# Optimization experiments

Measured on AMD Instinct MI355X. Metric: run time of the kernel, lower is better.

Reference implementation:

```python
import jax, jax.numpy as jnp
import numpy as np

N, E, R, F, HD = 4096, 2048, 4, 128, 256
DEG_EPS = 1e-8
BN_EPS = 1e-5
LN_EPS = 1e-5


def _xavier(k, shape):
    scale = np.sqrt(2.0 / (shape[-2] + shape[-1])).astype(np.float32)
    return jax.random.normal(k, shape, jnp.float32) * scale


def setup_inputs() -> dict:
    key = jax.random.key(0)
    ks = jax.random.split(key, 8)
    X = jax.random.normal(ks[0], (N, F), jnp.float32)
    # sparse binary incidence matrices, one per relation type, stacked [R,N,E]
    H = (jax.random.uniform(ks[1], (R, N, E)) < 0.05).astype(jnp.float32)
    return {
        "X": X,
        "H": H,
        "W1": _xavier(ks[2], (R, F, HD)),
        "W2": _xavier(ks[3], (R, HD, HD)),
        "W3": _xavier(ks[4], (R, HD, F)),
        "imp": jnp.ones((3, R), jnp.float32),        # relation_importance per conv layer
        "b1": jnp.zeros((HD,), jnp.float32),
        "b2": jnp.zeros((HD,), jnp.float32),
        "b3": jnp.zeros((F,), jnp.float32),
        "bn_gamma": jnp.ones((2, HD), jnp.float32),
        "bn_beta": jnp.zeros((2, HD), jnp.float32),
        "ln_gamma": jnp.ones((2, HD), jnp.float32),
        "ln_beta": jnp.zeros((2, HD), jnp.float32),
        "rel_attn": jnp.ones((R,), jnp.float32) / R,
    }


def typed_conv(X, Hw, W, imp, bias):
    # Hw: [R,N,E] weighted incidence; theta = Dv^{-1/2} H De^{-1/2} via row/col scaling
    dv = jnp.power(Hw.sum(axis=2) + DEG_EPS, -0.5)   # [R,N]
    de = jnp.power(Hw.sum(axis=1) + DEG_EPS, -0.5)   # [R,E]
    theta = Hw * dv[:, :, None] * de[:, None, :]     # [R,N,E]
    # (theta @ theta^T) @ X computed as theta @ (theta^T @ X) -- same math, no NxN
    t = jnp.einsum('rne,nf->ref', theta, X)          # [R,E,Fin]
    Hn = jnp.einsum('rne,ref->rnf', theta, t)        # [R,N,Fin]
    out = jnp.einsum('rnf,rfo->rno', Hn, W)          # [R,N,Fout]
    out = out * jax.nn.sigmoid(imp)[:, None, None]
    return out.sum(axis=0) + bias


def bn_ln_elu(X, bg, bb, lg, lb):
    # BatchNorm1d with batch statistics (biased var), then LayerNorm, then ELU
    mu = X.mean(axis=0)
    var = X.var(axis=0)
    X = (X - mu) * jax.lax.rsqrt(var + BN_EPS) * bg + bb
    m = X.mean(axis=-1, keepdims=True)
    v = X.var(axis=-1, keepdims=True)
    X = (X - m) * jax.lax.rsqrt(v + LN_EPS) * lg + lb
    return jax.nn.elu(X)


def reference(X, H, W1, W2, W3, imp, b1, b2, b3, bn_gamma, bn_beta, ln_gamma, ln_beta, rel_attn):
    rw = jax.nn.softmax(rel_attn)
    Hw = H * rw[:, None, None]                       # weighted incidence per relation
    h = typed_conv(X, Hw, W1, imp[0], b1)
    h = bn_ln_elu(h, bn_gamma[0], bn_beta[0], ln_gamma[0], ln_beta[0])
    h = typed_conv(h, Hw, W2, imp[1], b2)
    h = bn_ln_elu(h, bn_gamma[1], bn_beta[1], ln_gamma[1], ln_beta[1])
    out = typed_conv(h, Hw, W3, imp[2], b3)
    return out + X  # residual: out_channels == in_channels by construction
```

## Files before the change

kernel.cpp:

```cpp
#include <hip/hip_runtime.h>
#include <hip/hip_bf16.h>

#define NN 4096
#define EE 2048
#define RR 4
#define FF 128
#define HDD 256

typedef __attribute__((ext_vector_type(4))) float floatx4;
typedef __attribute__((ext_vector_type(8))) __bf16 bf16x8;

#define AS1 __attribute__((address_space(1)))
#define AS3 __attribute__((address_space(3)))

__device__ __forceinline__ void async16(const void* g, void* l) {
  __builtin_amdgcn_global_load_lds((const AS1 void*)(unsigned long long)(g),
                                   (AS3 void*)(unsigned int)(unsigned long long)(l),
                                   16, 0, 0);
}

__device__ inline unsigned short f2b(float x) {
  unsigned int u = __float_as_uint(x);
  unsigned int r = u + 0x7fffu + ((u >> 16) & 1u);
  return (unsigned short)(r >> 16);
}
__device__ inline float b2f(unsigned short u) { return __uint_as_float((unsigned int)u << 16); }

__device__ inline float rel_w(const float* rel, int r) {
  float m = fmaxf(fmaxf(rel[0], rel[1]), fmaxf(rel[2], rel[3]));
  float s = 0.f;
#pragma unroll
  for (int i = 0; i < RR; i++) s += expf(rel[i] - m);
  return expf(rel[r] - m) / s;
}

__global__ void k_dvmask(const float* __restrict__ H, const float* __restrict__ rel,
                         float* __restrict__ dvs, unsigned long long* __restrict__ mask) {
  int wave = (blockIdx.x << 2) | (threadIdx.x >> 6);
  int lane = threadIdx.x & 63;
  int r = wave >> 12;
  const float* row = H + (size_t)wave * EE;
  unsigned long long* mrow = mask + (size_t)wave * (EE / 64);
  float s = 0.f;
  for (int j = 0; j < EE / 64; j++) {
    float h = row[j * 64 + lane];
    s += h;
    unsigned long long m = __ballot(h != 0.0f);
    if (lane == 0) mrow[j] = m;
  }
  for (int off = 32; off; off >>= 1) s += __shfl_down(s, off);
  if (lane == 0) {
    float rwr = rel_w(rel, r);
    dvs[wave] = rwr * rsqrtf(rwr * s + 1e-8f);
  }
}

__global__ void k_de_pop(const unsigned long long* __restrict__ mask, float* __restrict__ de_acc) {
  int wid = threadIdx.x >> 6, lane = threadIdx.x & 63;
  int wcol = blockIdx.x, r = blockIdx.z;
  int n0 = (blockIdx.y << 8) + (wid << 6);
  unsigned long long w = mask[(size_t)(r * NN + n0 + lane) * (EE / 64) + wcol];
  float cnt = 0.f;
#pragma unroll
  for (int b = 0; b < 64; b++) {
    unsigned long long m = __ballot(((w >> b) & 1ULL) != 0);
    if (lane == b) cnt = (float)__popcll(m);
  }
  atomicAdd(&de_acc[r * EE + (wcol << 6) + lane], cnt);
}

__global__ void k_build_theta_bits(const unsigned long long* __restrict__ mask,
                                   const float* __restrict__ dvs, const float* __restrict__ decnt,
                                   const float* __restrict__ rel,
                                   unsigned short* __restrict__ theta, unsigned short* __restrict__ thetaT) {
  __shared__ unsigned short tile[64][65];
  int r = blockIdx.z;
  int e0 = blockIdx.x * 64, n0 = blockIdx.y * 64;
  int tr = threadIdx.x >> 4, tc = threadIdx.x & 15;
  float rwr = rel_w(rel, r);
  float de0 = rsqrtf(rwr * decnt[r * EE + e0 + tc * 4 + 0] + 1e-8f);
  float de1 = rsqrtf(rwr * decnt[r * EE + e0 + tc * 4 + 1] + 1e-8f);
  float de2 = rsqrtf(rwr * decnt[r * EE + e0 + tc * 4 + 2] + 1e-8f);
  float de3 = rsqrtf(rwr * decnt[r * EE + e0 + tc * 4 + 3] + 1e-8f);
  int wcol = e0 >> 6;
#pragma unroll
  for (int i = 0; i < 4; i++) {
    int n = n0 + tr + 16 * i;
    unsigned long long w = mask[((size_t)r * NN + n) * (EE / 64) + wcol];
    float d = dvs[r * NN + n];
    unsigned short b0 = ((w >> (tc * 4 + 0)) & 1) ? f2b(d * de0) : 0;
    unsigned short b1 = ((w >> (tc * 4 + 1)) & 1) ? f2b(d * de1) : 0;
    unsigned short b2 = ((w >> (tc * 4 + 2)) & 1) ? f2b(d * de2) : 0;
    unsigned short b3 = ((w >> (tc * 4 + 3)) & 1) ? f2b(d * de3) : 0;
    ushort4 o; o.x = b0; o.y = b1; o.z = b2; o.w = b3;
    *(ushort4*)(theta + ((size_t)r * NN + n) * EE + e0 + tc * 4) = o;
    tile[tr + 16 * i][tc * 4 + 0] = b0;
    tile[tr + 16 * i][tc * 4 + 1] = b1;
    tile[tr + 16 * i][tc * 4 + 2] = b2;
    tile[tr + 16 * i][tc * 4 + 3] = b3;
  }
  __syncthreads();
#pragma unroll
  for (int i = 0; i < 4; i++) {
    int e = e0 + tr + 16 * i;
    ushort4 o;
    o.x = tile[tc * 4 + 0][tr + 16 * i];
    o.y = tile[tc * 4 + 1][tr + 16 * i];
    o.z = tile[tc * 4 + 2][tr + 16 * i];
    o.w = tile[tc * 4 + 3][tr + 16 * i];
    *(ushort4*)(thetaT + ((size_t)r * EE + e) * NN + n0 + tc * 4) = o;
  }
}

__global__ void k_cvtT(const float* __restrict__ src, unsigned short* __restrict__ dst, int M, int C) {
  __shared__ unsigned short tile[64][65];
  int c0 = blockIdx.x * 64, m0 = blockIdx.y * 64;
  int tr = threadIdx.x >> 4, tc = threadIdx.x & 15;
#pragma unroll
  for (int i = 0; i < 4; i++) {
    int m = m0 + tr + 16 * i;
    float4 v = *(const float4*)(src + (size_t)m * C + c0 + tc * 4);
    tile[tr + 16 * i][tc * 4 + 0] = f2b(v.x);
    tile[tr + 16 * i][tc * 4 + 1] = f2b(v.y);
    tile[tr + 16 * i][tc * 4 + 2] = f2b(v.z);
    tile[tr + 16 * i][tc * 4 + 3] = f2b(v.w);
  }
  __syncthreads();
#pragma unroll
  for (int i = 0; i < 4; i++) {
    int c = c0 + tr + 16 * i;
    ushort4 v;
    v.x = tile[tc * 4 + 0][tr + 16 * i];
    v.y = tile[tc * 4 + 1][tr + 16 * i];
    v.z = tile[tc * 4 + 2][tr + 16 * i];
    v.w = tile[tc * 4 + 3][tr + 16 * i];
    *(ushort4*)(dst + (size_t)c * M + m0 + tc * 4) = v;
  }
}

__global__ void k_trz(const unsigned short* __restrict__ src, unsigned short* __restrict__ dst, int M, int C) {
  __shared__ unsigned short tile[64][65];
  int c0 = blockIdx.x * 64, m0 = blockIdx.y * 64;
  int tr = threadIdx.x >> 4, tc = threadIdx.x & 15;
#pragma unroll
  for (int i = 0; i < 4; i++) {
    int m = m0 + tr + 16 * i;
    ushort4 v = *(const ushort4*)(src + (size_t)m * C + c0 + tc * 4);
    tile[tr + 16 * i][tc * 4 + 0] = v.x;
    tile[tr + 16 * i][tc * 4 + 1] = v.y;
    tile[tr + 16 * i][tc * 4 + 2] = v.z;
    tile[tr + 16 * i][tc * 4 + 3] = v.w;
  }
  __syncthreads();
#pragma unroll
  for (int i = 0; i < 4; i++) {
    int c = c0 + tr + 16 * i;
    ushort4 v;
    v.x = tile[tc * 4 + 0][tr + 16 * i];
    v.y = tile[tc * 4 + 1][tr + 16 * i];
    v.z = tile[tc * 4 + 2][tr + 16 * i];
    v.w = tile[tc * 4 + 3][tr + 16 * i];
    *(ushort4*)(dst + (size_t)c * M + m0 + tc * 4) = v;
  }
}

__global__ void k_wprep(const float* __restrict__ W1, const float* __restrict__ W2,
                        const float* __restrict__ W3, const float* __restrict__ imp,
                        unsigned short* __restrict__ W1catT, unsigned short* __restrict__ W2T,
                        unsigned short* __restrict__ W3T) {
  int idx = blockIdx.x * 256 + threadIdx.x;
  if (idx < RR * FF * HDD) {
    int o = idx % HDD, f = (idx / HDD) % FF, r = idx / (HDD * FF);
    float sg = 1.0f / (1.0f + expf(-imp[r]));
    W1catT[(size_t)o * (RR * FF) + r * FF + f] = f2b(sg * W1[((size_t)r * FF + f) * HDD + o]);
  } else if (idx < RR * FF * HDD + RR * HDD * HDD) {
    int j = idx - RR * FF * HDD;
    int c = j % HDD, o = (j / HDD) % HDD, r = j / (HDD * HDD);
    float sg = 1.0f / (1.0f + expf(-imp[RR + r]));
    W2T[j] = f2b(sg * W2[((size_t)r * HDD + c) * HDD + o]);
  } else {
    int j = idx - RR * FF * HDD - RR * HDD * HDD;
    int c = j % HDD, o = (j / HDD) % FF, r = j / (HDD * FF);
    float sg = 1.0f / (1.0f + expf(-imp[2 * RR + r]));
    W3T[j] = f2b(sg * W3[((size_t)r * HDD + c) * FF + o]);
  }
}

__global__ __launch_bounds__(256) void k_gemm3(
    const unsigned short* __restrict__ A, const unsigned short* __restrict__ BT,
    int K, int SK, int lda, int ldb, long a_rs, long b_rs,
    unsigned short* __restrict__ P, long c_ps, int ldc) {
  __shared__ unsigned short Al[128 * 64];
  __shared__ unsigned short Bl[128 * 64];
  int tid = threadIdx.x, wid = tid >> 6, lane = tid & 63;
  int m0 = blockIdx.x << 7, n0 = blockIdx.y << 7;
  int z = blockIdx.z, zr = z / SK, kz = z - zr * SK;
  int Kc = K / SK;
  int r8 = lane >> 3, c8 = lane & 7;
  int swz = ((c8 ^ r8) << 3);
  const unsigned short* Ab = A + (size_t)zr * a_rs + (size_t)m0 * lda + (size_t)kz * Kc;
  const unsigned short* Bb = BT + (size_t)zr * b_rs + (size_t)n0 * ldb + (size_t)kz * Kc;
  int wm = (wid >> 1) << 6, wn = (wid & 1) << 6;
  int fm = lane & 15, quad = lane >> 4;
  int f7 = fm & 7;
  floatx4 acc[4][4];
#pragma unroll
  for (int i = 0; i < 4; i++)
#pragma unroll
    for (int j = 0; j < 4; j++) acc[i][j] = (floatx4){0.f, 0.f, 0.f, 0.f};
  for (int k0 = 0; k0 < Kc; k0 += 64) {
#pragma unroll
    for (int t = 0; t < 4; t++) {
      int rbase = (wid << 5) + (t << 3);
      int row = rbase + r8;
      async16(Ab + (size_t)row * lda + k0 + swz, &Al[rbase * 64 + lane * 8]);
      async16(Bb + (size_t)row * ldb + k0 + swz, &Bl[rbase * 64 + lane * 8]);
    }
    __syncthreads();
#pragma unroll
    for (int ks = 0; ks < 2; ks++) {
      int kg = (ks << 2) | quad;
      int ko = ((kg ^ f7) << 3);
      bf16x8 a[4], b[4];
#pragma unroll
      for (int i = 0; i < 4; i++) {
        a[i] = *(const bf16x8*)&Al[(wm + i * 16 + fm) * 64 + ko];
        b[i] = *(const bf16x8*)&Bl[(wn + i * 16 + fm) * 64 + ko];
      }
#pragma unroll
      for (int i = 0; i < 4; i++)
#pragma unroll
        for (int j = 0; j < 4; j++)
          acc[i][j] = __builtin_amdgcn_mfma_f32_16x16x32_bf16(a[i], b[j], acc[i][j], 0, 0, 0);
    }
    __syncthreads();
  }
  unsigned short* Cb = P + (size_t)z * c_ps;
#pragma unroll
  for (int mi = 0; mi < 4; mi++)
#pragma unroll
    for (int ni = 0; ni < 4; ni++)
#pragma unroll
      for (int v = 0; v < 4; v++) {
        int row = m0 + wm + mi * 16 + quad * 4 + v;
        int col = n0 + wn + ni * 16 + fm;
        Cb[(size_t)row * ldc + col] = f2b(acc[mi][ni][v]);
      }
}

__global__ void k_red_b(const unsigned short* __restrict__ P, unsigned short* __restrict__ out,
                        int SK, long region) {
  long i = ((long)blockIdx.x * 256 + threadIdx.x) * 8;
  int zr = blockIdx.y;
  const unsigned short* p = P + (size_t)zr * SK * region + i;
  float s[8] = {0, 0, 0, 0, 0, 0, 0, 0};
  for (int k = 0; k < SK; k++) {
    const unsigned short* q = p + (size_t)k * region;
    ushort4 a = *(const ushort4*)q;
    ushort4 b = *(const ushort4*)(q + 4);
    s[0] += b2f(a.x); s[1] += b2f(a.y); s[2] += b2f(a.z); s[3] += b2f(a.w);
    s[4] += b2f(b.x); s[5] += b2f(b.y); s[6] += b2f(b.z); s[7] += b2f(b.w);
  }
  ushort4 o0, o1;
  o0.x = f2b(s[0]); o0.y = f2b(s[1]); o0.z = f2b(s[2]); o0.w = f2b(s[3]);
  o1.x = f2b(s[4]); o1.y = f2b(s[5]); o1.z = f2b(s[6]); o1.w = f2b(s[7]);
  unsigned short* d = out + (size_t)zr * region + i;
  *(ushort4*)d = o0;
  *(ushort4*)(d + 4) = o1;
}

__global__ void k_redT_b(const unsigned short* __restrict__ P, unsigned short* __restrict__ outT,
                         int SK, int M, int C) {
  __shared__ unsigned short tile[64][65];
  int zr = blockIdx.z;
  long region = (long)M * C;
  const unsigned short* p0 = P + (size_t)zr * SK * region;
  int c0 = blockIdx.x * 64, m0 = blockIdx.y * 64;
  int tr = threadIdx.x >> 4, tc = threadIdx.x & 15;
#pragma unroll
  for (int i = 0; i < 4; i++) {
    int m = m0 + tr + 16 * i;
    const unsigned short* p = p0 + (size_t)m * C + c0 + tc * 4;
    float s0 = 0, s1 = 0, s2 = 0, s3 = 0;
    for (int k = 0; k < SK; k++) {
      ushort4 v = *(const ushort4*)(p + (size_t)k * region);
      s0 += b2f(v.x); s1 += b2f(v.y); s2 += b2f(v.z); s3 += b2f(v.w);
    }
    tile[tr + 16 * i][tc * 4 + 0] = f2b(s0);
    tile[tr + 16 * i][tc * 4 + 1] = f2b(s1);
    tile[tr + 16 * i][tc * 4 + 2] = f2b(s2);
    tile[tr + 16 * i][tc * 4 + 3] = f2b(s3);
  }
  __syncthreads();
  unsigned short* d = outT + (size_t)zr * region;
#pragma unroll
  for (int i = 0; i < 4; i++) {
    int c = c0 + tr + 16 * i;
    ushort4 v;
    v.x = tile[tc * 4 + 0][tr + 16 * i];
    v.y = tile[tc * 4 + 1][tr + 16 * i];
    v.z = tile[tc * 4 + 2][tr + 16 * i];
    v.w = tile[tc * 4 + 3][tr + 16 * i];
    *(ushort4*)(d + (size_t)c * M + m0 + tc * 4) = v;
  }
}

__global__ void k_red_hcatb(const unsigned short* __restrict__ P, unsigned short* __restrict__ out, int SK) {
  long i = ((long)blockIdx.x * 256 + threadIdx.x) * 8;
  int r = blockIdx.y;
  const unsigned short* p = P + (size_t)r * SK * (NN * FF) + i;
  float s[8] = {0, 0, 0, 0, 0, 0, 0, 0};
  for (int k = 0; k < SK; k++) {
    const unsigned short* q = p + (size_t)k * (NN * FF);
    ushort4 a = *(const ushort4*)q;
    ushort4 b = *(const ushort4*)(q + 4);
    s[0] += b2f(a.x); s[1] += b2f(a.y); s[2] += b2f(a.z); s[3] += b2f(a.w);
    s[4] += b2f(b.x); s[5] += b2f(b.y); s[6] += b2f(b.z); s[7] += b2f(b.w);
  }
  long n = i >> 7;
  int f = (int)(i & 127);
  ushort4 o0, o1;
  o0.x = f2b(s[0]); o0.y = f2b(s[1]); o0.z = f2b(s[2]); o0.w = f2b(s[3]);
  o1.x = f2b(s[4]); o1.y = f2b(s[5]); o1.z = f2b(s[6]); o1.w = f2b(s[7]);
  unsigned short* d = out + n * (RR * FF) + r * FF + f;
  *(ushort4*)d = o0;
  *(ushort4*)(d + 4) = o1;
}

__global__ void k_redstats(const unsigned short* __restrict__ P, float* __restrict__ out,
                           float* __restrict__ cs, float* __restrict__ cs2, int Z) {
  __shared__ float sm[2][8][256];
  int cg = (threadIdx.x & 31) << 3;
  int rowt = threadIdx.x >> 5;
  int r0 = blockIdx.x * 32;
  float s[8] = {0, 0, 0, 0, 0, 0, 0, 0}, s2[8] = {0, 0, 0, 0, 0, 0, 0, 0};
  for (int j = 0; j < 4; j++) {
    long idx = (long)(r0 + rowt * 4 + j) * HDD + cg;
    float acc[8] = {0, 0, 0, 0, 0, 0, 0, 0};
    for (int z = 0; z < Z; z++) {
      const unsigned short* p = P + (size_t)z * ((long)NN * HDD) + idx;
      ushort4 a = *(const ushort4*)p;
      ushort4 b = *(const ushort4*)(p + 4);
      acc[0] += b2f(a.x); acc[1] += b2f(a.y); acc[2] += b2f(a.z); acc[3] += b2f(a.w);
      acc[4] += b2f(b.x); acc[5] += b2f(b.y); acc[6] += b2f(b.z); acc[7] += b2f(b.w);
    }
    float4 o0 = {acc[0], acc[1], acc[2], acc[3]};
    float4 o1 = {acc[4], acc[5], acc[6], acc[7]};
    *(float4*)(out + idx) = o0;
    *(float4*)(out + idx + 4) = o1;
#pragma unroll
    for (int i = 0; i < 8; i++) { s[i] += acc[i]; s2[i] += acc[i] * acc[i]; }
  }
#pragma unroll
  for (int i = 0; i < 8; i++) { sm[0][rowt][cg + i] = s[i]; sm[1][rowt][cg + i] = s2[i]; }
  __syncthreads();
  int c = threadIdx.x;
  float a0 = 0, a1 = 0;
#pragma unroll
  for (int t = 0; t < 8; t++) { a0 += sm[0][t][c]; a1 += sm[1][t][c]; }
  atomicAdd(&cs[c], a0);
  atomicAdd(&cs2[c], a1);
}

__global__ void k_red_out(const unsigned short* __restrict__ P, const float* __restrict__ X,
                          const float* __restrict__ b3, float* __restrict__ out, int Z) {
  long i = ((long)blockIdx.x * 256 + threadIdx.x) * 4;
  int f = (int)(i & 127);
  float4 s = *(const float4*)(X + i);
  s.x += b3[f]; s.y += b3[f + 1]; s.z += b3[f + 2]; s.w += b3[f + 3];
  for (int z = 0; z < Z; z++) {
    ushort4 v = *(const ushort4*)(P + (size_t)z * (NN * FF) + i);
    s.x += b2f(v.x); s.y += b2f(v.y); s.z += b2f(v.z); s.w += b2f(v.w);
  }
  *(float4*)(out + i) = s;
}

__global__ void k_bnlnelu(const float* __restrict__ x, const float* __restrict__ cs, const float* __restrict__ cs2,
                          const float* __restrict__ bg, const float* __restrict__ bb,
                          const float* __restrict__ lg, const float* __restrict__ lb,
                          unsigned short* __restrict__ out) {
  int wid = threadIdx.x >> 6, lane = threadIdx.x & 63;
  int n = blockIdx.x * 4 + wid;
  float y[4];
  float m = 0.f;
#pragma unroll
  for (int j = 0; j < 4; j++) {
    int c = lane + 64 * j;
    float mu = cs[c] * (1.0f / NN);
    float var = cs2[c] * (1.0f / NN) - mu * mu;
    float xv = x[(size_t)n * HDD + c];
    y[j] = (xv - mu) * rsqrtf(var + 1e-5f) * bg[c] + bb[c];
    m += y[j];
  }
  for (int off = 32; off; off >>= 1) m += __shfl_down(m, off);
  m = __shfl(m, 0) * (1.0f / HDD);
  float var = 0.f;
#pragma unroll
  for (int j = 0; j < 4; j++) { float d = y[j] - m; var += d * d; }
  for (int off = 32; off; off >>= 1) var += __shfl_down(var, off);
  var = __shfl(var, 0) * (1.0f / HDD);
  float inv = rsqrtf(var + 1e-5f);
#pragma unroll
  for (int j = 0; j < 4; j++) {
    int c = lane + 64 * j;
    float z = (y[j] - m) * inv * lg[c] + lb[c];
    z = z > 0.f ? z : expm1f(z);
    out[(size_t)n * HDD + c] = f2b(z);
  }
}

extern "C" void kernel_launch(void* const* d_in, const int* in_sizes, int n_in,
                              void* d_out, int out_size, void* d_ws, size_t ws_size,
                              hipStream_t stream) {
  const float* X   = (const float*)d_in[0];
  const float* H   = (const float*)d_in[1];
  const float* W1  = (const float*)d_in[2];
  const float* W2  = (const float*)d_in[3];
  const float* W3  = (const float*)d_in[4];
  const float* imp = (const float*)d_in[5];
  const float* b3  = (const float*)d_in[8];
  const float* bng = (const float*)d_in[9];
  const float* bnb = (const float*)d_in[10];
  const float* lng = (const float*)d_in[11];
  const float* lnb = (const float*)d_in[12];
  const float* rel = (const float*)d_in[13];
  (void)in_sizes; (void)n_in; (void)out_size; (void)ws_size;

  char* w = (char*)d_ws;
  size_t off = 0;
  auto alloc = [&](size_t bytes) -> void* {
    void* p = w + off;
    off += (bytes + 255) & ~(size_t)255;
    return p;
  };
  float* dvs  = (float*)alloc((size_t)RR * NN * 4);
  float* de   = (float*)alloc((size_t)RR * EE * 4);
  float* cs   = (float*)alloc(2 * HDD * 4);
  unsigned long long* mask = (unsigned long long*)alloc((size_t)RR * NN * (EE / 64) * 8);
  unsigned short* theta  = (unsigned short*)alloc((size_t)RR * NN * EE * 2);
  unsigned short* thetaT = (unsigned short*)alloc((size_t)RR * NN * EE * 2);
  unsigned short* bufP = (unsigned short*)alloc((size_t)16 * NN * HDD * 2);
  unsigned short* bufC = (unsigned short*)alloc((size_t)RR * EE * HDD * 2);
  unsigned short* bufD = (unsigned short*)alloc((size_t)RR * EE * HDD * 2);
  unsigned short* bufE = (unsigned short*)alloc((size_t)RR * EE * HDD * 2);
  float* convout = (float*)alloc((size_t)NN * HDD * 4);
  unsigned short* Xb  = (unsigned short*)alloc((size_t)NN * HDD * 2);
  unsigned short* XbT = (unsigned short*)alloc((size_t)NN * HDD * 2);
  unsigned short* W1catT = (unsigned short*)alloc((size_t)RR * FF * HDD * 2);
  unsigned short* W2T    = (unsigned short*)alloc((size_t)RR * HDD * HDD * 2);
  unsigned short* W3T    = (unsigned short*)alloc((size_t)RR * HDD * FF * 2);

  k_dvmask<<<(RR * NN) / 4, 256, 0, stream>>>(H, rel, dvs, mask);
  hipMemsetAsync(de, 0, (size_t)RR * EE * 4, stream);
  k_de_pop<<<dim3(EE / 64, NN / 256, RR), 256, 0, stream>>>(mask, de);
  k_build_theta_bits<<<dim3(EE / 64, NN / 64, RR), 256, 0, stream>>>(mask, dvs, de, rel, theta, thetaT);
  k_cvtT<<<dim3(FF / 64, NN / 64), 256, 0, stream>>>(X, XbT, NN, FF);
  k_wprep<<<(RR * FF * HDD + RR * HDD * HDD + RR * HDD * FF) / 256, 256, 0, stream>>>(
      W1, W2, W3, imp, W1catT, W2T, W3T);

  k_gemm3<<<dim3(1, EE / 128, RR * 8), 256, 0, stream>>>(
      XbT, thetaT, NN, 8, NN, NN, 0, (long)EE * NN, bufP, (long)FF * EE, EE);
  k_red_b<<<dim3((FF * EE) / 2048, RR), 256, 0, stream>>>(bufP, bufC, 8, (long)FF * EE);
  k_gemm3<<<dim3(NN / 128, 1, RR * 2), 256, 0, stream>>>(
      theta, bufC, EE, 2, EE, EE, (long)NN * EE, (long)FF * EE, bufP, (long)NN * FF, FF);
  k_red_hcatb<<<dim3((NN * FF) / 2048, RR), 256, 0, stream>>>(bufP, bufD, 2);
  k_gemm3<<<dim3(NN / 128, HDD / 128, 4), 256, 0, stream>>>(
      bufD, W1catT, RR * FF, 4, RR * FF, RR * FF, 0, 0, bufP, (long)NN * HDD, HDD);
  hipMemsetAsync(cs, 0, 2 * HDD * 4, stream);
  k_redstats<<<NN / 32, 256, 0, stream>>>(bufP, convout, cs, cs + HDD, 4);
  k_bnlnelu<<<NN / 4, 256, 0, stream>>>(convout, cs, cs + HDD, bng, bnb, lng, lnb, Xb);
  k_trz<<<dim3(HDD / 64, NN / 64), 256, 0, stream>>>(Xb, XbT, NN, HDD);

  k_gemm3<<<dim3(64, HDD / 128, 4), 256, 0, stream>>>(
      thetaT, XbT, NN, 4, NN, NN, 0, 0, bufP, (long)RR * EE * HDD, HDD);
  k_red_b<<<dim3((RR * EE * HDD) / 2048, 1), 256, 0, stream>>>(bufP, bufD, 4, (long)RR * EE * HDD);
  k_gemm3<<<dim3(EE / 128, HDD / 128, RR * 2), 256, 0, stream>>>(
      bufD, W2T, HDD, 2, HDD, HDD, (long)EE * HDD, (long)HDD * HDD, bufP, (long)EE * HDD, HDD);
  k_redT_b<<<dim3(HDD / 64, EE / 64, RR), 256, 0, stream>>>(bufP, bufE, 2, EE, HDD);
  k_gemm3<<<dim3(NN / 128, HDD / 128, RR * 2), 256, 0, stream>>>(
      theta, bufE, EE, 2, EE, EE, (long)NN * EE, (long)HDD * EE, bufP, (long)NN * HDD, HDD);
  hipMemsetAsync(cs, 0, 2 * HDD * 4, stream);
  k_redstats<<<NN / 32, 256, 0, stream>>>(bufP, convout, cs, cs + HDD, 8);
  k_bnlnelu<<<NN / 4, 256, 0, stream>>>(convout, cs, cs + HDD, bng + HDD, bnb + HDD, lng + HDD, lnb + HDD, Xb);

  k_gemm3<<<dim3(NN / 128, 1, RR * 2), 256, 0, stream>>>(
      Xb, W3T, HDD, 2, HDD, HDD, 0, (long)FF * HDD, bufP, (long)NN * FF, FF);
  k_redT_b<<<dim3(FF / 64, NN / 64, RR), 256, 0, stream>>>(bufP, bufD, 2, NN, FF);
  k_gemm3<<<dim3(EE / 128, 1, RR * 4), 256, 0, stream>>>(
      thetaT, bufD, NN, 4, NN, NN, (long)EE * NN, (long)FF * NN, bufP, (long)EE * FF, FF);
  k_redT_b<<<dim3(FF / 64, EE / 64, RR), 256, 0, stream>>>(bufP, bufE, 4, EE, FF);
  k_gemm3<<<dim3(NN / 128, 1, RR * 2), 256, 0, stream>>>(
      theta, bufE, EE, 2, EE, EE, (long)NN * EE, (long)FF * EE, bufP, (long)NN * FF, FF);
  k_red_out<<<(NN * FF) / 1024, 256, 0, stream>>>(bufP, X, b3, (float*)d_out, 8);
}
```

Measured before the change: 506.1 us.

## Swap GEMM operand order to emit transposed outputs and drop transpose-reduce kernels

Layers 2 and 3 now compute the weight products with swapped operands (W^T·X^T style), so each GEMM writes its result already in the transposed layout the next GEMM needs. The split-K partials for the small-K W2/W3 products are removed (SK=1), which eliminates three k_redT_b transpose-reduction launches and their partial-buffer traffic. Layer 3 reorders its work so the reduction after the thetaT GEMM becomes a plain k_red_b into bufC. The trade-off is less split-K parallelism in those GEMMs and grids with fewer blocks.

```diff
diff --git a/kernel.cpp b/kernel.cpp
--- a/kernel.cpp
+++ b/kernel.cpp
@@ -267,42 +267,6 @@
   unsigned short* d = out + (size_t)zr * region + i;
   *(ushort4*)d = o0;
   *(ushort4*)(d + 4) = o1;
-}
-
-__global__ void k_redT_b(const unsigned short* __restrict__ P, unsigned short* __restrict__ outT,
-                         int SK, int M, int C) {
-  __shared__ unsigned short tile[64][65];
-  int zr = blockIdx.z;
-  long region = (long)M * C;
-  const unsigned short* p0 = P + (size_t)zr * SK * region;
-  int c0 = blockIdx.x * 64, m0 = blockIdx.y * 64;
-  int tr = threadIdx.x >> 4, tc = threadIdx.x & 15;
-#pragma unroll
-  for (int i = 0; i < 4; i++) {
-    int m = m0 + tr + 16 * i;
-    const unsigned short* p = p0 + (size_t)m * C + c0 + tc * 4;
-    float s0 = 0, s1 = 0, s2 = 0, s3 = 0;
-    for (int k = 0; k < SK; k++) {
-      ushort4 v = *(const ushort4*)(p + (size_t)k * region);
-      s0 += b2f(v.x); s1 += b2f(v.y); s2 += b2f(v.z); s3 += b2f(v.w);
-    }
-    tile[tr + 16 * i][tc * 4 + 0] = f2b(s0);
-    tile[tr + 16 * i][tc * 4 + 1] = f2b(s1);
-    tile[tr + 16 * i][tc * 4 + 2] = f2b(s2);
-    tile[tr + 16 * i][tc * 4 + 3] = f2b(s3);
-  }
-  __syncthreads();
-  unsigned short* d = outT + (size_t)zr * region;
-#pragma unroll
-  for (int i = 0; i < 4; i++) {
-    int c = c0 + tr + 16 * i;
-    ushort4 v;
-    v.x = tile[tc * 4 + 0][tr + 16 * i];
-    v.y = tile[tc * 4 + 1][tr + 16 * i];
-    v.z = tile[tc * 4 + 2][tr + 16 * i];
-    v.w = tile[tc * 4 + 3][tr + 16 * i];
-    *(ushort4*)(d + (size_t)c * M + m0 + tc * 4) = v;
-  }
 }
 
 __global__ void k_red_hcatb(const unsigned short* __restrict__ P, unsigned short* __restrict__ out, int SK) {
@@ -474,22 +438,20 @@
   k_gemm3<<<dim3(64, HDD / 128, 4), 256, 0, stream>>>(
       thetaT, XbT, NN, 4, NN, NN, 0, 0, bufP, (long)RR * EE * HDD, HDD);
   k_red_b<<<dim3((RR * EE * HDD) / 2048, 1), 256, 0, stream>>>(bufP, bufD, 4, (long)RR * EE * HDD);
-  k_gemm3<<<dim3(EE / 128, HDD / 128, RR * 2), 256, 0, stream>>>(
-      bufD, W2T, HDD, 2, HDD, HDD, (long)EE * HDD, (long)HDD * HDD, bufP, (long)EE * HDD, HDD);
-  k_redT_b<<<dim3(HDD / 64, EE / 64, RR), 256, 0, stream>>>(bufP, bufE, 2, EE, HDD);
+  k_gemm3<<<dim3(HDD / 128, EE / 128, RR), 256, 0, stream>>>(
+      W2T, bufD, HDD, 1, HDD, HDD, (long)HDD * HDD, (long)EE * HDD, bufE, (long)HDD * EE, EE);
   k_gemm3<<<dim3(NN / 128, HDD / 128, RR * 2), 256, 0, stream>>>(
       theta, bufE, EE, 2, EE, EE, (long)NN * EE, (long)HDD * EE, bufP, (long)NN * HDD, HDD);
   hipMemsetAsync(cs, 0, 2 * HDD * 4, stream);
   k_redstats<<<NN / 32, 256, 0, stream>>>(bufP, convout, cs, cs + HDD, 8);
   k_bnlnelu<<<NN / 4, 256, 0, stream>>>(convout, cs, cs + HDD, bng + HDD, bnb + HDD, lng + HDD, lnb + HDD, Xb);
 
+  k_gemm3<<<dim3(1, NN / 128, RR), 256, 0, stream>>>(
+      W3T, Xb, HDD, 1, HDD, HDD, (long)FF * HDD, 0, bufD, (long)FF * NN, NN);
+  k_gemm3<<<dim3(1, EE / 128, RR * 4), 256, 0, stream>>>(
+      bufD, thetaT, NN, 4, NN, NN, (long)FF * NN, (long)EE * NN, bufP, (long)FF * EE, EE);
+  k_red_b<<<dim3((FF * EE) / 2048, RR), 256, 0, stream>>>(bufP, bufC, 4, (long)FF * EE);
   k_gemm3<<<dim3(NN / 128, 1, RR * 2), 256, 0, stream>>>(
-      Xb, W3T, HDD, 2, HDD, HDD, 0, (long)FF * HDD, bufP, (long)NN * FF, FF);
-  k_redT_b<<<dim3(FF / 64, NN / 64, RR), 256, 0, stream>>>(bufP, bufD, 2, NN, FF);
-  k_gemm3<<<dim3(EE / 128, 1, RR * 4), 256, 0, stream>>>(
-      thetaT, bufD, NN, 4, NN, NN, (long)EE * NN, (long)FF * NN, bufP, (long)EE * FF, FF);
-  k_redT_b<<<dim3(FF / 64, EE / 64, RR), 256, 0, stream>>>(bufP, bufE, 4, EE, FF);
-  k_gemm3<<<dim3(NN / 128, 1, RR * 2), 256, 0, stream>>>(
-      theta, bufE, EE, 2, EE, EE, (long)NN * EE, (long)FF * EE, bufP, (long)NN * FF, FF);
+      theta, bufC, EE, 2, EE, EE, (long)NN * EE, (long)FF * EE, bufP, (long)NN * FF, FF);
   k_red_out<<<(NN * FF) / 1024, 256, 0, stream>>>(bufP, X, b3, (float*)d_out, 8);
 }
```

After: 488.2 us (median of 2 runs). 3.5% less time.
